# Kernel optimization log

Hardware: AMD Instinct MI355X
Metric: run time of the kernel (lower is better)

The kernel has to match this reference:

```python
import jax, jax.numpy as jnp
import numpy as np

N_NODES = 50000
N_FEAT = 256
HIDDEN = 256
N_EDGES = 800000


def gcn_conv(x, edge_index, W, b):
    """PyG GCNConv: out = D^-1/2 (A+I) D^-1/2 (x @ W) + b."""
    n = x.shape[0]
    loop = jnp.arange(n, dtype=edge_index.dtype)
    src = jnp.concatenate([edge_index[0], loop])  # [E+N]
    dst = jnp.concatenate([edge_index[1], loop])  # [E+N]
    deg = jax.ops.segment_sum(jnp.ones_like(dst, dtype=x.dtype), dst, num_segments=n)
    dinv = jnp.where(deg > 0, jax.lax.rsqrt(deg), 0.0)
    norm = dinv[src] * dinv[dst]                  # [E+N]
    h = x @ W                                     # [N, out]
    msg = h[src] * norm[:, None]                  # gather + scale
    out = jax.ops.segment_sum(msg, dst, num_segments=n)  # scatter-add
    return out + b


def setup_inputs() -> dict:
    key = jax.random.key(0)
    ks = jax.random.split(key, 8)
    x = jax.random.normal(ks[0], (N_NODES, N_FEAT), dtype=jnp.float32)
    train_pos_edge_index = jax.random.randint(ks[1], (2, N_EDGES), 0, N_NODES, dtype=jnp.int64)
    pos_edge_index = jax.random.randint(ks[2], (2, N_EDGES), 0, N_NODES, dtype=jnp.int64)
    neg_edge_index = jax.random.randint(ks[3], (2, N_EDGES), 0, N_NODES, dtype=jnp.int64)
    # Glorot-style init for GCN weights
    W1 = jax.random.normal(ks[4], (N_FEAT, HIDDEN), dtype=jnp.float32) * (1.0 / np.sqrt(N_FEAT))
    b1 = jnp.zeros((HIDDEN,), dtype=jnp.float32)
    W2 = jax.random.normal(ks[5], (HIDDEN, HIDDEN // 2), dtype=jnp.float32) * (1.0 / np.sqrt(HIDDEN))
    b2 = jnp.zeros((HIDDEN // 2,), dtype=jnp.float32)
    return {"x": x, "train_pos_edge_index": train_pos_edge_index,
            "pos_edge_index": pos_edge_index, "neg_edge_index": neg_edge_index,
            "W1": W1, "b1": b1, "W2": W2, "b2": b2}


def reference(x, train_pos_edge_index, pos_edge_index, neg_edge_index, W1, b1, W2, b2):
    # encode
    h = jax.nn.relu(gcn_conv(x, train_pos_edge_index, W1, b1))
    z = gcn_conv(h, train_pos_edge_index, W2, b2)  # [N, HIDDEN//2]
    # decode: dot product over concatenated pos+neg edges
    edge_index = jnp.concatenate([pos_edge_index, neg_edge_index], axis=-1)  # [2, 2E]
    logits = jnp.sum(z[edge_index[0]] * z[edge_index[1]], axis=-1)           # [2E]
    return logits
```

## Files before the change

kernel.cpp:

```cpp
#include <hip/hip_runtime.h>
#include <hip/hip_fp16.h>


#define NFEAT 256
#define HID   256
#define OUTF  128

typedef _Float16 f16x8 __attribute__((ext_vector_type(8)));
typedef _Float16 f16x2 __attribute__((ext_vector_type(2)));
typedef float    f32x4 __attribute__((ext_vector_type(4)));

__global__ void k_init_deg(float* __restrict__ deg, int n) {
    int i = blockIdx.x * blockDim.x + threadIdx.x;
    if (i < n) deg[i] = 1.0f;
}

__global__ void k_count_deg(const int* __restrict__ ei, float* __restrict__ deg, int E) {
    int e = blockIdx.x * blockDim.x + threadIdx.x;
    if (e < E) atomicAdd(&deg[ei[E + e]], 1.0f);
}

__global__ __launch_bounds__(1024) void k_scan1(
        const float* __restrict__ deg, int* __restrict__ excl,
        int* __restrict__ bsum, int n) {
    __shared__ int swsum[16];
    const int t = threadIdx.x, wave = t >> 6, lane = t & 63;
    const int i = blockIdx.x * 1024 + t;
    int v = (i < n) ? (int)deg[i] - 1 : 0;
    int sc = v;
#pragma unroll
    for (int off = 1; off < 64; off <<= 1) {
        int y = __shfl_up(sc, off);
        if (lane >= off) sc += y;
    }
    if (lane == 63) swsum[wave] = sc;
    __syncthreads();
    if (t < 16) {
        int w = swsum[t];
        int scw = w;
#pragma unroll
        for (int off = 1; off < 16; off <<= 1) {
            int y = __shfl_up(scw, off);
            if (t >= off) scw += y;
        }
        swsum[t] = scw - w;
        if (t == 15) bsum[blockIdx.x] = scw;
    }
    __syncthreads();
    if (i < n) excl[i] = swsum[wave] + (sc - v);
}

__global__ void k_scan2(int* __restrict__ bsum, int nb) {
    int t = threadIdx.x;
    int v = (t < nb) ? bsum[t] : 0;
    int sc = v;
#pragma unroll
    for (int off = 1; off < 64; off <<= 1) {
        int y = __shfl_up(sc, off);
        if (t >= off) sc += y;
    }
    if (t < nb) bsum[t] = sc - v;
    if (t == 63) bsum[nb] = sc;
}

__global__ void k_scan3(float* __restrict__ deg_dinv, const int* __restrict__ excl,
                        const int* __restrict__ bsum, int* __restrict__ rowptr,
                        int* __restrict__ cursor, int n, int nb) {
    int i = blockIdx.x * blockDim.x + threadIdx.x;
    if (i < n) {
        int rp = excl[i] + bsum[i >> 10];
        rowptr[i] = rp;
        cursor[i] = rp;
        deg_dinv[i] = rsqrtf(deg_dinv[i]);
    } else if (i == n) {
        rowptr[n] = bsum[nb];
    }
}

__global__ void k_fill(const int* __restrict__ ei, int* __restrict__ cursor,
                       int* __restrict__ eidx, int E) {
    int e = blockIdx.x * blockDim.x + threadIdx.x;
    if (e < E) {
        int s = ei[e];
        int d = ei[E + e];
        int p = atomicAdd(&cursor[d], 1);
        eidx[p] = s;
    }
}

__global__ __launch_bounds__(256) void k_wt(const float* __restrict__ W,
                                            __half* __restrict__ Wt, int K, int M) {
    __shared__ float tile[32][33];
    int k0 = blockIdx.x * 32, m0 = blockIdx.y * 32;
    int tx = threadIdx.x & 31, ty = threadIdx.x >> 5;
#pragma unroll
    for (int r = 0; r < 4; ++r)
        tile[ty + r * 8][tx] = W[(size_t)(k0 + ty + r * 8) * M + m0 + tx];
    __syncthreads();
#pragma unroll
    for (int r = 0; r < 4; ++r)
        Wt[(size_t)(m0 + ty + r * 8) * K + k0 + tx] = __float2half(tile[tx][ty + r * 8]);
}

template <int MT, bool AF32, int SWL>
__global__ __launch_bounds__(256) void k_gemm_mfma(
        const void* __restrict__ Aptr, const __half* __restrict__ Wt,
        const float* __restrict__ dinv, __half* __restrict__ outp,
        int n, int K, int M) {
    constexpr int BM = 2 * MT * 16;
    __shared__ __half As[BM][40];
    __shared__ __half Bs[128][40];
    __shared__ __half Cs[4][16][72];

    const int t    = threadIdx.x;
    const int wave = t >> 6;
    const int lane = t & 63;
    const int row0 = blockIdx.x * BM;
    const int col0 = blockIdx.y * 128;
    const int wm = wave >> 1, wn = wave & 1;
    const int lr = lane & 15;
    const int kq = lane >> 4;

    f32x4 acc[MT][4];
#pragma unroll
    for (int i = 0; i < MT; ++i)
#pragma unroll
        for (int j = 0; j < 4; ++j) acc[i][j] = (f32x4){0.f, 0.f, 0.f, 0.f};

    for (int k0 = 0; k0 < K; k0 += 32) {
        if (AF32) {
            const float* A = (const float*)Aptr;
#pragma unroll
            for (int it = 0; it < BM * 8 / 256; ++it) {
                int q = t + it * 256;
                int r = q >> 3, c4 = q & 7;
                int gr = min(row0 + r, n - 1);
                float4 v = *(const float4*)&A[(size_t)gr * K + k0 + c4 * 4];
                __half2* dst = (__half2*)&As[r][c4 * 4];
                dst[0] = __floats2half2_rn(v.x, v.y);
                dst[1] = __floats2half2_rn(v.z, v.w);
            }
        } else {
            const __half* A = (const __half*)Aptr;
#pragma unroll
            for (int it = 0; it < BM * 4 / 256; ++it) {
                int q = t + it * 256;
                int r = q >> 2, c8 = q & 3;
                int gr = min(row0 + r, n - 1);
                *(float4*)&As[r][c8 * 8] = *(const float4*)&A[(size_t)gr * K + k0 + c8 * 8];
            }
        }
#pragma unroll
        for (int it = 0; it < 2; ++it) {
            int q = t + it * 256;
            int r = q >> 2, c8 = q & 3;
            *(float4*)&Bs[r][c8 * 8] = *(const float4*)&Wt[(size_t)(col0 + r) * K + k0 + c8 * 8];
        }
        __syncthreads();

        f16x8 b[4];
#pragma unroll
        for (int j = 0; j < 4; ++j)
            b[j] = *(const f16x8*)&Bs[wn * 64 + j * 16 + lr][kq * 8];
#pragma unroll
        for (int i = 0; i < MT; ++i) {
            f16x8 a = *(const f16x8*)&As[wm * MT * 16 + i * 16 + lr][kq * 8];
#pragma unroll
            for (int j = 0; j < 4; ++j)
                acc[i][j] = __builtin_amdgcn_mfma_f32_16x16x32_f16(a, b[j], acc[i][j], 0, 0, 0);
        }
        __syncthreads();
    }

    constexpr int SW = 1 << SWL;
#pragma unroll
    for (int i = 0; i < MT; ++i) {
        int gr0 = row0 + wm * MT * 16 + i * 16;
        float dv[4];
#pragma unroll
        for (int r = 0; r < 4; ++r)
            dv[r] = dinv[min(gr0 + kq * 4 + r, n - 1)];
        __syncthreads();
#pragma unroll
        for (int j = 0; j < 4; ++j)
#pragma unroll
            for (int r = 0; r < 4; ++r)
                Cs[wave][kq * 4 + r][j * 16 + lr] = __float2half(acc[i][j][r] * dv[r]);
        __syncthreads();
        int r1 = lane >> 3, c1 = (lane & 7) * 8;
#pragma unroll
        for (int h = 0; h < 2; ++h) {
            int grow = gr0 + r1 + h * 8;
            if (grow < n) {
                int col = col0 + wn * 64 + c1;
                size_t oidx = ((size_t)(col >> SWL) * n + grow) * SW + (col & (SW - 1));
                *(float4*)&outp[oidx] = *(const float4*)&Cs[wave][r1 + h * 8][c1];
            }
        }
    }
}

__global__ __launch_bounds__(256) void k_agg1(
        const int* __restrict__ rowptr, const int* __restrict__ eidx,
        const __half* __restrict__ g, const float* __restrict__ dinv,
        const float* __restrict__ bias, __half* __restrict__ out, int n) {
    const int node = (int)(((size_t)blockIdx.x * blockDim.x + threadIdx.x) >> 6);
    const int lane = threadIdx.x & 63;
    const int half = lane >> 5;
    const int fl   = lane & 31;
    if (node >= n) return;
    const int j0  = rowptr[node];
    const int end = rowptr[node + 1];
    const int last = end - 1;

    union U { float4 f; __half2 h[4]; };
    float acc[8] = {0.f, 0.f, 0.f, 0.f, 0.f, 0.f, 0.f, 0.f};
    {
        if (half == 0) {
            U u; u.f = *(const float4*)&g[(size_t)node * HID + fl * 8];
#pragma unroll
            for (int k = 0; k < 4; ++k) {
                float2 v = __half22float2(u.h[k]);
                acc[k * 2] += v.x; acc[k * 2 + 1] += v.y;
            }
        }
    }
    if (j0 < end) {
        int s0 = eidx[min(j0 + half, last)];
        int s1 = eidx[min(j0 + 2 + half, last)];
        for (int j = j0; j < end; j += 4) {
            int p0 = eidx[min(j + 4 + half, last)];
            int p1 = eidx[min(j + 6 + half, last)];
            U u0, u1;
            u0.f = *(const float4*)&g[(size_t)s0 * HID + fl * 8];
            u1.f = *(const float4*)&g[(size_t)s1 * HID + fl * 8];
            if (j + half < end) {
#pragma unroll
                for (int k = 0; k < 4; ++k) {
                    float2 v = __half22float2(u0.h[k]);
                    acc[k * 2] += v.x; acc[k * 2 + 1] += v.y;
                }
            }
            if (j + 2 + half < end) {
#pragma unroll
                for (int k = 0; k < 4; ++k) {
                    float2 v = __half22float2(u1.h[k]);
                    acc[k * 2] += v.x; acc[k * 2 + 1] += v.y;
                }
            }
            s0 = p0; s1 = p1;
        }
    }
#pragma unroll
    for (int k = 0; k < 8; ++k) acc[k] += __shfl_xor(acc[k], 32);
    if (half == 0) {
        const float sc = dinv[node];
        const int f0 = fl * 8;
        U r;
#pragma unroll
        for (int k = 0; k < 4; ++k) {
            float2 bb = *(const float2*)&bias[f0 + k * 2];
            r.h[k] = __floats2half2_rn(fmaxf(sc * acc[k * 2]     + bb.x, 0.f),
                                       fmaxf(sc * acc[k * 2 + 1] + bb.y, 0.f));
        }
        *(float4*)&out[(size_t)node * HID + f0] = r.f;
    }
}

__global__ __launch_bounds__(256) void k_agg2(
        const int* __restrict__ rowptr, const int* __restrict__ eidx,
        const __half* __restrict__ g, const float* __restrict__ dinv,
        const float* __restrict__ bias, __half* __restrict__ zs, int n) {
    const int node = (int)(((size_t)blockIdx.x * blockDim.x + threadIdx.x) >> 6);
    const int lane = threadIdx.x & 63;
    const int q    = lane >> 4;
    const int fl   = lane & 15;
    if (node >= n) return;
    const int j0  = rowptr[node];
    const int end = rowptr[node + 1];
    const int last = end - 1;

    union U { float4 f; __half2 h[4]; };
    float acc[8] = {0.f, 0.f, 0.f, 0.f, 0.f, 0.f, 0.f, 0.f};
    if (q == 0) {
        U u; u.f = *(const float4*)&g[(size_t)node * OUTF + fl * 8];
#pragma unroll
        for (int k = 0; k < 4; ++k) {
            float2 v = __half22float2(u.h[k]);
            acc[k * 2] += v.x; acc[k * 2 + 1] += v.y;
        }
    }
    if (j0 < end) {
        int s0 = eidx[min(j0 + q, last)];
        for (int j = j0; j < end; j += 4) {
            int p0 = eidx[min(j + 4 + q, last)];
            U u0; u0.f = *(const float4*)&g[(size_t)s0 * OUTF + fl * 8];
            if (j + q < end) {
#pragma unroll
                for (int k = 0; k < 4; ++k) {
                    float2 v = __half22float2(u0.h[k]);
                    acc[k * 2] += v.x; acc[k * 2 + 1] += v.y;
                }
            }
            s0 = p0;
        }
    }
#pragma unroll
    for (int k = 0; k < 8; ++k) {
        acc[k] += __shfl_xor(acc[k], 16);
        acc[k] += __shfl_xor(acc[k], 32);
    }
    if (q == 0) {
        const float sc = dinv[node];
        const int f0 = fl * 8;
        U r;
#pragma unroll
        for (int k = 0; k < 4; ++k) {
            float2 bb = *(const float2*)&bias[f0 + k * 2];
            r.h[k] = __floats2half2_rn(sc * acc[k * 2]     + bb.x,
                                       sc * acc[k * 2 + 1] + bb.y);
        }
        *(float4*)&zs[((size_t)(f0 >> 5) * n + node) * 32 + (f0 & 31)] = r.f;
    }
}

__global__ __launch_bounds__(256) void k_decode(
        const int* __restrict__ pos, const int* __restrict__ neg,
        const __half* __restrict__ zs, float* __restrict__ psum, int E, int n) {
    const int slice = blockIdx.x & 3;
    const int wv    = threadIdx.x >> 6;
    const int lane  = threadIdx.x & 63;
    const int eo    = lane >> 1;
    const int h     = lane & 1;
    int e = ((blockIdx.x >> 2) * 4 + wv) * 32 + eo;
    if (e >= 2 * E) return;
    int a, b;
    if (e < E) { a = pos[e];     b = pos[E + e]; }
    else       { a = neg[e - E]; b = neg[e];     }
    const __half* ra = zs + ((size_t)slice * n + a) * 32 + h * 16;
    const __half* rb = zs + ((size_t)slice * n + b) * 32 + h * 16;
    union U { float4 f; f16x2 d[4]; };
    U a0, a1, b0, b1;
    a0.f = *(const float4*)&ra[0];
    a1.f = *(const float4*)&ra[8];
    b0.f = *(const float4*)&rb[0];
    b1.f = *(const float4*)&rb[8];
    float p = 0.f;
#if __has_builtin(__builtin_amdgcn_fdot2)
#pragma unroll
    for (int k = 0; k < 4; ++k) p = __builtin_amdgcn_fdot2(a0.d[k], b0.d[k], p, false);
#pragma unroll
    for (int k = 0; k < 4; ++k) p = __builtin_amdgcn_fdot2(a1.d[k], b1.d[k], p, false);
#else
#pragma unroll
    for (int k = 0; k < 4; ++k) {
        p += (float)a0.d[k][0] * (float)b0.d[k][0] + (float)a0.d[k][1] * (float)b0.d[k][1];
        p += (float)a1.d[k][0] * (float)b1.d[k][0] + (float)a1.d[k][1] * (float)b1.d[k][1];
    }
#endif
    p += __shfl_xor(p, 1);
    if (h == 0)
        __builtin_nontemporal_store(p, &psum[(size_t)slice * 2 * E + e]);
}

__global__ void k_dsum(const float* __restrict__ psum, float* __restrict__ out, int n2e) {
    int e = blockIdx.x * blockDim.x + threadIdx.x;
    if (e < n2e) {
        float p0 = __builtin_nontemporal_load(&psum[e]);
        float p1 = __builtin_nontemporal_load(&psum[(size_t)n2e + e]);
        float p2 = __builtin_nontemporal_load(&psum[2 * (size_t)n2e + e]);
        float p3 = __builtin_nontemporal_load(&psum[3 * (size_t)n2e + e]);
        out[e] = (p0 + p1) + (p2 + p3);
    }
}

extern "C" void kernel_launch(void* const* d_in, const int* in_sizes, int n_in,
                              void* d_out, int out_size, void* d_ws, size_t ws_size,
                              hipStream_t stream) {
    const float* x   = (const float*)d_in[0];
    const int*   tei = (const int*)d_in[1];
    const int*   pos = (const int*)d_in[2];
    const int*   neg = (const int*)d_in[3];
    const float* W1  = (const float*)d_in[4];
    const float* b1  = (const float*)d_in[5];
    const float* W2  = (const float*)d_in[6];
    const float* b2  = (const float*)d_in[7];
    float* out = (float*)d_out;

    const int N = in_sizes[0] / NFEAT;
    const int E = in_sizes[1] / 2;
    const int NB = (N + 1023) / 1024;

    char* ws = (char*)d_ws;
    size_t off = 0;
    __half* g1h = (__half*)(ws + off);
    __half* g2h = (__half*)(ws + off);
    __half* zs  = (__half*)(ws + off + (size_t)N * OUTF * 2);
    off += (size_t)N * HID * 2;
    __half* h1h  = (__half*)(ws + off);
    float*  psum = (float*)(ws + off);
    off += (size_t)N * HID * 2;
    float*  dinv = (float*)(ws + off);  off += (size_t)N * 4;
    int* rowptr = (int*)(ws + off);     off += (size_t)(N + 1) * 4;
    int* cursor = (int*)(ws + off);     off += (size_t)N * 4;
    int* eidx   = (int*)(ws + off);     off += (size_t)E * 4;
    __half* W1t = (__half*)(ws + off);  off += (size_t)NFEAT * HID * 2;
    __half* W2t = (__half*)(ws + off);  off += (size_t)HID * OUTF * 2;
    int* excl   = (int*)(ws + off);     off += (size_t)N * 4;
    int* bsum   = (int*)(ws + off);     off += (size_t)(NB + 1) * 4;

    { dim3 g(NFEAT / 32, HID / 32);  k_wt<<<g, 256, 0, stream>>>(W1, W1t, NFEAT, HID); }
    { dim3 g(HID / 32, OUTF / 32);   k_wt<<<g, 256, 0, stream>>>(W2, W2t, HID, OUTF); }

    k_init_deg<<<(N + 255) / 256, 256, 0, stream>>>(dinv, N);
    k_count_deg<<<(E + 255) / 256, 256, 0, stream>>>(tei, dinv, E);
    k_scan1<<<NB, 1024, 0, stream>>>(dinv, excl, bsum, N);
    k_scan2<<<1, 64, 0, stream>>>(bsum, NB);
    k_scan3<<<(N + 256) / 256, 256, 0, stream>>>(dinv, excl, bsum, rowptr, cursor, N, NB);
    k_fill<<<(E + 255) / 256, 256, 0, stream>>>(tei, cursor, eidx, E);

    {
        dim3 grid((N + 127) / 128, HID / 128);
        k_gemm_mfma<4, true, 8><<<grid, 256, 0, stream>>>(x, W1t, dinv, g1h, N, NFEAT, HID);
        int nblk = (int)(((size_t)N * 64 + 255) / 256);
        k_agg1<<<nblk, 256, 0, stream>>>(rowptr, eidx, g1h, dinv, b1, h1h, N);
    }

    {
        dim3 grid((N + 63) / 64, OUTF / 128);
        k_gemm_mfma<2, false, 7><<<grid, 256, 0, stream>>>(h1h, W2t, dinv, g2h, N, HID, OUTF);
        int nblk = (int)(((size_t)N * 64 + 255) / 256);
        k_agg2<<<nblk, 256, 0, stream>>>(rowptr, eidx, g2h, dinv, b2, zs, N);
    }

    {
        int nblk = 4 * ((2 * E + 127) / 128);
        k_decode<<<nblk, 256, 0, stream>>>(pos, neg, zs, psum, E, N);
        k_dsum<<<(2 * E + 255) / 256, 256, 0, stream>>>(psum, out, 2 * E);
    }
}
```

Before: 406.8 us.

## Slice GEMM outputs into 32-column panels and aggregate per slice

The GEMMs now write their outputs in 32-feature column slices (SWL=5), and a single templated aggregation kernel replaces agg1/agg2. Each block handles one slice for four nodes, with 16 edges in parallel per wave and 4 lanes per 64-byte row. The goal is to shrink the gathered working set per pass so it stays cache-resident, which should cut DRAM traffic from random neighbor gathers. The cost is rereading eidx once per slice and launching more blocks, and the old index prefetching is gone.

```diff
diff --git a/kernel.cpp b/kernel.cpp
--- a/kernel.cpp
+++ b/kernel.cpp
@@ -200,24 +200,25 @@
     }
 }
 
-__global__ __launch_bounds__(256) void k_agg1(
+template <int S, bool RELU, bool OUT_SLICED>
+__global__ __launch_bounds__(256) void k_aggs(
         const int* __restrict__ rowptr, const int* __restrict__ eidx,
-        const __half* __restrict__ g, const float* __restrict__ dinv,
+        const __half* __restrict__ gsl, const float* __restrict__ dinv,
         const float* __restrict__ bias, __half* __restrict__ out, int n) {
-    const int node = (int)(((size_t)blockIdx.x * blockDim.x + threadIdx.x) >> 6);
-    const int lane = threadIdx.x & 63;
-    const int half = lane >> 5;
-    const int fl   = lane & 31;
+    const int slice = blockIdx.x & (S - 1);
+    const int node  = (blockIdx.x / S) * 4 + (threadIdx.x >> 6);
+    const int lane  = threadIdx.x & 63;
+    const int es    = lane >> 2;
+    const int fl    = lane & 3;
     if (node >= n) return;
-    const int j0  = rowptr[node];
-    const int end = rowptr[node + 1];
-    const int last = end - 1;
+    const __half* base = gsl + (size_t)slice * n * 32;
+    const int j0 = rowptr[node], end = rowptr[node + 1];
 
     union U { float4 f; __half2 h[4]; };
     float acc[8] = {0.f, 0.f, 0.f, 0.f, 0.f, 0.f, 0.f, 0.f};
     {
-        if (half == 0) {
-            U u; u.f = *(const float4*)&g[(size_t)node * HID + fl * 8];
+        U u; u.f = *(const float4*)&base[(size_t)node * 32 + fl * 8];
+        if (es == 0) {
 #pragma unroll
             for (int k = 0; k < 4; ++k) {
                 float2 v = __half22float2(u.h[k]);
@@ -226,101 +227,39 @@
         }
     }
     if (j0 < end) {
-        int s0 = eidx[min(j0 + half, last)];
-        int s1 = eidx[min(j0 + 2 + half, last)];
-        for (int j = j0; j < end; j += 4) {
-            int p0 = eidx[min(j + 4 + half, last)];
-            int p1 = eidx[min(j + 6 + half, last)];
-            U u0, u1;
-            u0.f = *(const float4*)&g[(size_t)s0 * HID + fl * 8];
-            u1.f = *(const float4*)&g[(size_t)s1 * HID + fl * 8];
-            if (j + half < end) {
+        const int last = end - 1;
+        for (int j = j0; j < end; j += 16) {
+            int s = eidx[min(j + es, last)];
+            U u; u.f = *(const float4*)&base[(size_t)s * 32 + fl * 8];
+            if (j + es < end) {
 #pragma unroll
                 for (int k = 0; k < 4; ++k) {
-                    float2 v = __half22float2(u0.h[k]);
+                    float2 v = __half22float2(u.h[k]);
                     acc[k * 2] += v.x; acc[k * 2 + 1] += v.y;
                 }
             }
-            if (j + 2 + half < end) {
-#pragma unroll
-                for (int k = 0; k < 4; ++k) {
-                    float2 v = __half22float2(u1.h[k]);
-                    acc[k * 2] += v.x; acc[k * 2 + 1] += v.y;
-                }
-            }
-            s0 = p0; s1 = p1;
-        }
-    }
-#pragma unroll
-    for (int k = 0; k < 8; ++k) acc[k] += __shfl_xor(acc[k], 32);
-    if (half == 0) {
+        }
+    }
+#pragma unroll
+    for (int m = 4; m <= 32; m <<= 1)
+#pragma unroll
+        for (int k = 0; k < 8; ++k) acc[k] += __shfl_xor(acc[k], m);
+    if (es == 0) {
         const float sc = dinv[node];
-        const int f0 = fl * 8;
+        const int f0 = slice * 32 + fl * 8;
         U r;
 #pragma unroll
         for (int k = 0; k < 4; ++k) {
             float2 bb = *(const float2*)&bias[f0 + k * 2];
-            r.h[k] = __floats2half2_rn(fmaxf(sc * acc[k * 2]     + bb.x, 0.f),
-                                       fmaxf(sc * acc[k * 2 + 1] + bb.y, 0.f));
-        }
-        *(float4*)&out[(size_t)node * HID + f0] = r.f;
-    }
-}
-
-__global__ __launch_bounds__(256) void k_agg2(
-        const int* __restrict__ rowptr, const int* __restrict__ eidx,
-        const __half* __restrict__ g, const float* __restrict__ dinv,
-        const float* __restrict__ bias, __half* __restrict__ zs, int n) {
-    const int node = (int)(((size_t)blockIdx.x * blockDim.x + threadIdx.x) >> 6);
-    const int lane = threadIdx.x & 63;
-    const int q    = lane >> 4;
-    const int fl   = lane & 15;
-    if (node >= n) return;
-    const int j0  = rowptr[node];
-    const int end = rowptr[node + 1];
-    const int last = end - 1;
-
-    union U { float4 f; __half2 h[4]; };
-    float acc[8] = {0.f, 0.f, 0.f, 0.f, 0.f, 0.f, 0.f, 0.f};
-    if (q == 0) {
-        U u; u.f = *(const float4*)&g[(size_t)node * OUTF + fl * 8];
-#pragma unroll
-        for (int k = 0; k < 4; ++k) {
-            float2 v = __half22float2(u.h[k]);
-            acc[k * 2] += v.x; acc[k * 2 + 1] += v.y;
-        }
-    }
-    if (j0 < end) {
-        int s0 = eidx[min(j0 + q, last)];
-        for (int j = j0; j < end; j += 4) {
-            int p0 = eidx[min(j + 4 + q, last)];
-            U u0; u0.f = *(const float4*)&g[(size_t)s0 * OUTF + fl * 8];
-            if (j + q < end) {
-#pragma unroll
-                for (int k = 0; k < 4; ++k) {
-                    float2 v = __half22float2(u0.h[k]);
-                    acc[k * 2] += v.x; acc[k * 2 + 1] += v.y;
-                }
-            }
-            s0 = p0;
-        }
-    }
-#pragma unroll
-    for (int k = 0; k < 8; ++k) {
-        acc[k] += __shfl_xor(acc[k], 16);
-        acc[k] += __shfl_xor(acc[k], 32);
-    }
-    if (q == 0) {
-        const float sc = dinv[node];
-        const int f0 = fl * 8;
-        U r;
-#pragma unroll
-        for (int k = 0; k < 4; ++k) {
-            float2 bb = *(const float2*)&bias[f0 + k * 2];
-            r.h[k] = __floats2half2_rn(sc * acc[k * 2]     + bb.x,
-                                       sc * acc[k * 2 + 1] + bb.y);
-        }
-        *(float4*)&zs[((size_t)(f0 >> 5) * n + node) * 32 + (f0 & 31)] = r.f;
+            float vx = sc * acc[k * 2]     + bb.x;
+            float vy = sc * acc[k * 2 + 1] + bb.y;
+            if (RELU) { vx = fmaxf(vx, 0.f); vy = fmaxf(vy, 0.f); }
+            r.h[k] = __floats2half2_rn(vx, vy);
+        }
+        if (OUT_SLICED)
+            *(float4*)&out[((size_t)slice * n + node) * 32 + fl * 8] = r.f;
+        else
+            *(float4*)&out[(size_t)node * (S * 32) + f0] = r.f;
     }
 }
 
@@ -393,8 +332,8 @@
 
     char* ws = (char*)d_ws;
     size_t off = 0;
-    __half* g1h = (__half*)(ws + off);
-    __half* g2h = (__half*)(ws + off);
+    __half* g1s = (__half*)(ws + off);
+    __half* g2s = (__half*)(ws + off);
     __half* zs  = (__half*)(ws + off + (size_t)N * OUTF * 2);
     off += (size_t)N * HID * 2;
     __half* h1h  = (__half*)(ws + off);
@@ -421,16 +360,16 @@
 
     {
         dim3 grid((N + 127) / 128, HID / 128);
-        k_gemm_mfma<4, true, 8><<<grid, 256, 0, stream>>>(x, W1t, dinv, g1h, N, NFEAT, HID);
-        int nblk = (int)(((size_t)N * 64 + 255) / 256);
-        k_agg1<<<nblk, 256, 0, stream>>>(rowptr, eidx, g1h, dinv, b1, h1h, N);
+        k_gemm_mfma<4, true, 5><<<grid, 256, 0, stream>>>(x, W1t, dinv, g1s, N, NFEAT, HID);
+        int nblk = 8 * ((N + 3) / 4);
+        k_aggs<8, true, false><<<nblk, 256, 0, stream>>>(rowptr, eidx, g1s, dinv, b1, h1h, N);
     }
 
     {
         dim3 grid((N + 63) / 64, OUTF / 128);
-        k_gemm_mfma<2, false, 7><<<grid, 256, 0, stream>>>(h1h, W2t, dinv, g2h, N, HID, OUTF);
-        int nblk = (int)(((size_t)N * 64 + 255) / 256);
-        k_agg2<<<nblk, 256, 0, stream>>>(rowptr, eidx, g2h, dinv, b2, zs, N);
+        k_gemm_mfma<2, false, 5><<<grid, 256, 0, stream>>>(h1h, W2t, dinv, g2s, N, HID, OUTF);
+        int nblk = 4 * ((N + 3) / 4);
+        k_aggs<4, false, true><<<nblk, 256, 0, stream>>>(rowptr, eidx, g2s, dinv, b2, zs, N);
     }
 
     {
```

Measured after the change: 522.9 us. +28.5%, slower.
